# Kernel tuning notes

Hardware: AMD Instinct MI355X
Metric: run time of the kernel (lower is better)

## Reference

```python
import jax, jax.numpy as jnp
import numpy as np

N_NODES = 100000
LATENT_DIM = 8
SAMPLE_SIZE = 8192
N_EDGES = 1000000
EPS = 1e-6


def setup_inputs() -> dict:
    key = jax.random.key(0)
    k1, k2, k3, k4, k5 = jax.random.split(key, 5)
    latent_Z = jax.random.normal(k1, (N_NODES, LATENT_DIM), dtype=jnp.float32)
    alpha = jax.random.normal(k2, (1,), dtype=jnp.float32)
    sample_idx = jax.random.randint(k3, (SAMPLE_SIZE,), 0, N_NODES, dtype=jnp.int64)
    sparse_sample_i = jax.random.randint(k4, (N_EDGES,), 0, N_NODES, dtype=jnp.int64)
    sparse_sample_j = jax.random.randint(k5, (N_EDGES,), 0, N_NODES, dtype=jnp.int64)
    return {"latent_Z": latent_Z, "alpha": alpha, "sample_idx": sample_idx,
            "sparse_sample_i": sparse_sample_i, "sparse_sample_j": sparse_sample_j}


def reference(latent_Z, alpha, sample_idx, sparse_sample_i, sparse_sample_j):
    # --- dense non-edge term over the sampled subgraph ---
    Zs = latent_Z[sample_idx]                              # [S, D]
    diff = Zs[:, None, :] - Zs[None, :, :] + EPS           # [S, S, D]
    dist = jnp.sqrt(jnp.sum(diff * diff, axis=-1))         # [S, S]
    mat = jnp.exp(-dist)                                   # [S, S]
    # original uses exp(ones) vectors in the matmul-with-ones trick -> factor e^2
    ones_exp_sq = jnp.exp(jnp.float32(1.0)) ** 2
    offdiag_sum = jnp.sum(mat) - jnp.sum(jnp.diagonal(mat))
    z_pdist1 = jnp.exp(alpha[0]) * 0.5 * ones_exp_sq * offdiag_sum
    # --- sparse positive-edge term ---
    ed = latent_Z[sparse_sample_i] - latent_Z[sparse_sample_j] + EPS  # [E, D]
    edist = jnp.sqrt(jnp.sum(ed * ed, axis=-1))                        # [E]
    z_pdist2 = jnp.sum(-edist + alpha[0])
    return z_pdist2 - z_pdist1
```

## Files before the change

kernel.cpp:

```cpp
#include <hip/hip_runtime.h>
#include <hip/hip_bf16.h>
#include <math.h>

#define NNODES   100000
#define S        8192
#define D        8
#define EPSF     1e-6f
#define LOG2E    1.442695040888963f
#define EPS_S    (LOG2E * EPSF)
#define NT2      256

#define ZHL_OFF  0
#define U_OFF    262144
#define V_OFF    294912
#define ZB_OFF   327680
#define BK_OFF   1928192

#define NSBLK    256
#define NDBLK    1024
#define NWPP     32
#define CH       6

typedef __attribute__((ext_vector_type(8)))  short short8_t;
typedef __attribute__((ext_vector_type(16))) float f32x16;

__device__ __forceinline__ float block_reduce_f(float v, float* sm) {
    #pragma unroll
    for (int off = 32; off > 0; off >>= 1) v += __shfl_down(v, off, 64);
    int lane = threadIdx.x & 63, wid = threadIdx.x >> 6;
    if (lane == 0) sm[wid] = v;
    __syncthreads();
    float s = 0.f;
    if (threadIdx.x == 0) {
        for (int w = 0; w < 4; ++w) s += sm[w];
    }
    return s;
}

__global__ __launch_bounds__(256) void gather_kernel(const float* __restrict__ Z,
                                                     const int* __restrict__ idx,
                                                     ushort* __restrict__ zhl,
                                                     float* __restrict__ u,
                                                     float* __restrict__ v,
                                                     ushort* __restrict__ zb16,
                                                     char* __restrict__ buckets) {
    int gid = blockIdx.x * 256 + threadIdx.x;

    if (blockIdx.x == 0 && threadIdx.x < 161) {
        *(double*)(buckets + threadIdx.x * 128) = 0.0;
    }

    if (gid < S) {
        int n = idx[gid];
        const float4* zp = (const float4*)(Z + (size_t)n * D);
        float4 a = zp[0], b = zp[1];
        float z[8] = { a.x, a.y, a.z, a.w, b.x, b.y, b.z, b.w };
        float ss = 0.f;
        short8_t h, l;
        #pragma unroll
        for (int k = 0; k < 8; ++k) {
            float zs = LOG2E * z[k];
            ss = fmaf(zs, zs, ss);
            __hip_bfloat16 hb = __float2bfloat16(zs);
            float hf = __bfloat162float(hb);
            __hip_bfloat16 lb = __float2bfloat16(zs - hf);
            h[k] = (short)__builtin_bit_cast(unsigned short, hb);
            l[k] = (short)__builtin_bit_cast(unsigned short, lb);
        }
        *(short8_t*)(zhl + (size_t)gid * 16)     = h;
        *(short8_t*)(zhl + (size_t)gid * 16 + 8) = l;
        u[gid] = ss + 8.f * EPS_S * EPS_S;
        v[gid] = ss;
    }

    if (gid < NNODES) {
        const float4* zp = (const float4*)(Z + (size_t)gid * D);
        float4 a = zp[0], b = zp[1];
        float z[8] = { a.x, a.y, a.z, a.w, b.x, b.y, b.z, b.w };
        short8_t o;
        #pragma unroll
        for (int k = 0; k < 8; ++k) {
            __hip_bfloat16 bb = __float2bfloat16(z[k]);
            o[k] = (short)__builtin_bit_cast(unsigned short, bb);
        }
        *(short8_t*)(zb16 + (size_t)gid * 8) = o;
    }
}

#define UNPACK8(u4, f)                                        \
    f[0] = __uint_as_float(u4.x << 16);                       \
    f[1] = __uint_as_float(u4.x & 0xffff0000u);               \
    f[2] = __uint_as_float(u4.y << 16);                       \
    f[3] = __uint_as_float(u4.y & 0xffff0000u);               \
    f[4] = __uint_as_float(u4.z << 16);                       \
    f[5] = __uint_as_float(u4.z & 0xffff0000u);               \
    f[6] = __uint_as_float(u4.w << 16);                       \
    f[7] = __uint_as_float(u4.w & 0xffff0000u);

__device__ __forceinline__ float edge_dist8(const uint4* __restrict__ zb,
                                            int4 ia0, int4 ia1, int4 ib0, int4 ib1) {
    int aidx[8] = { ia0.x, ia0.y, ia0.z, ia0.w, ia1.x, ia1.y, ia1.z, ia1.w };
    int bidx[8] = { ib0.x, ib0.y, ib0.z, ib0.w, ib1.x, ib1.y, ib1.z, ib1.w };
    uint4 ua[8], ub[8];
    #pragma unroll
    for (int q = 0; q < 8; ++q) { ua[q] = zb[aidx[q]]; ub[q] = zb[bidx[q]]; }
    float acc = 0.f;
    #pragma unroll
    for (int q = 0; q < 8; ++q) {
        float fa[8], fb[8];
        UNPACK8(ua[q], fa);
        UNPACK8(ub[q], fb);
        float s2 = 0.f;
        #pragma unroll
        for (int k = 0; k < 8; ++k) {
            float d = fa[k] - fb[k] + EPSF;
            s2 = fmaf(d, d, s2);
        }
        acc += __builtin_amdgcn_sqrtf(s2);
    }
    return acc;
}

__device__ __forceinline__ void dense_sweep32(const ushort* __restrict__ zhl,
                                              const float* __restrict__ v,
                                              short8_t afrag, const float4* u4,
                                              int ti, int tj0, int cnt, int c31,
                                              float& ax, float& ay, float& az, float& aw) {
    const ushort* bp0 = zhl + (size_t)c31 * 16;
    const float*  vp0 = v + c31;
    for (int t0 = 0; t0 < cnt; t0 += CH) {
        short8_t hh[CH], ll[CH];
        float    vv[CH];
        #pragma unroll
        for (int k = 0; k < CH; ++k) {
            int tk = t0 + k;
            int T  = tj0 + (tk < cnt ? tk : cnt - 1);
            hh[k] = *(const short8_t*)(bp0 + (size_t)T * 512);
            ll[k] = *(const short8_t*)(bp0 + (size_t)T * 512 + 8);
            vv[k] = vp0[T * 32];
        }
        int m = cnt - t0; if (m > CH) m = CH;
        #pragma unroll
        for (int k = 0; k < CH; ++k) {
            if (k < m) {
                float w = (tj0 + t0 + k == ti) ? 1.f : 2.f;
                f32x16 c = { 0.f, 0.f, 0.f, 0.f, 0.f, 0.f, 0.f, 0.f,
                             0.f, 0.f, 0.f, 0.f, 0.f, 0.f, 0.f, 0.f };
                c = __builtin_amdgcn_mfma_f32_32x32x16_bf16(afrag, hh[k], c, 0, 0, 0);
                c = __builtin_amdgcn_mfma_f32_32x32x16_bf16(afrag, ll[k], c, 0, 0, 0);
                #pragma unroll
                for (int q = 0; q < 4; ++q) {
                    float s0 = u4[q].x + vv[k], s1 = u4[q].y + vv[k];
                    float s2 = u4[q].z + vv[k], s3 = u4[q].w + vv[k];
                    float d0 = fmaf(c[4*q+0], -2.f, s0);
                    float d1 = fmaf(c[4*q+1], -2.f, s1);
                    float d2 = fmaf(c[4*q+2], -2.f, s2);
                    float d3 = fmaf(c[4*q+3], -2.f, s3);
                    ax = fmaf(w, __builtin_amdgcn_exp2f(-__builtin_amdgcn_sqrtf(__builtin_fabsf(d0))), ax);
                    ay = fmaf(w, __builtin_amdgcn_exp2f(-__builtin_amdgcn_sqrtf(__builtin_fabsf(d1))), ay);
                    az = fmaf(w, __builtin_amdgcn_exp2f(-__builtin_amdgcn_sqrtf(__builtin_fabsf(d2))), az);
                    aw = fmaf(w, __builtin_amdgcn_exp2f(-__builtin_amdgcn_sqrtf(__builtin_fabsf(d3))), aw);
                }
            }
        }
    }
}

__global__ __launch_bounds__(256) void fused_kernel(
        const ushort* __restrict__ zhl, const float* __restrict__ u,
        const float* __restrict__ v, const ushort* __restrict__ zb16,
        const int* __restrict__ ei, const int* __restrict__ ej, int ne,
        const float* __restrict__ alpha, char* __restrict__ buckets,
        float* __restrict__ out) {
    __shared__ float red[4];
    __shared__ unsigned composeFlag;
    int tid = threadIdx.x, bx = blockIdx.x;
    float s;

    if (bx < NSBLK) {
        const uint4* zb = (const uint4*)zb16;
        const int4* ei4 = (const int4*)ei;
        const int4* ej4 = (const int4*)ej;
        float acc = 0.f;
        int nchunk = ne >> 3;
        int stride = NSBLK * 256;
        int c = bx * 256 + tid;
        if (c < nchunk) {
            int4 ia0 = ei4[2*c], ia1 = ei4[2*c+1];
            int4 ib0 = ej4[2*c], ib1 = ej4[2*c+1];
            while (true) {
                int cn = c + stride;
                bool more = cn < nchunk;
                int4 na0, na1, nb0, nb1;
                if (more) {
                    na0 = ei4[2*cn]; na1 = ei4[2*cn+1];
                    nb0 = ej4[2*cn]; nb1 = ej4[2*cn+1];
                }
                acc += edge_dist8(zb, ia0, ia1, ib0, ib1);
                if (!more) break;
                ia0 = na0; ia1 = na1; ib0 = nb0; ib1 = nb1; c = cn;
            }
        }
        for (int e = (nchunk << 3) + bx * 256 + tid; e < ne; e += stride) {
            uint4 ua = zb[ei[e]];
            uint4 ub = zb[ej[e]];
            float fa[8], fb[8];
            UNPACK8(ua, fa);
            UNPACK8(ub, fb);
            float s2 = 0.f;
            #pragma unroll
            for (int k = 0; k < 8; ++k) {
                float d = fa[k] - fb[k] + EPSF;
                s2 = fmaf(d, d, s2);
            }
            acc += __builtin_amdgcn_sqrtf(s2);
        }
        s = block_reduce_f(acc, red);
    } else {
        int dbx  = bx - NSBLK;
        int wave = tid >> 6, lane = tid & 63;
        int g = lane >> 5, c31 = lane & 31;

        int p  = dbx >> 3;
        int wv = (dbx & 7) * 4 + wave;
        int k0 = (wv * 257) / NWPP;
        int k1 = ((wv + 1) * 257) / NWPP;
        int n1 = NT2 - p;

        float ax = 0.f, ay = 0.f, az = 0.f, aw = 0.f;

        int eA = k1 < n1 ? k1 : n1;
        if (k0 < eA) {
            int ti = p;
            short8_t afrag = *(const short8_t*)(zhl + (size_t)(ti * 32 + c31) * 16 + g * 8);
            float4 u4[4];
            #pragma unroll
            for (int q = 0; q < 4; ++q) u4[q] = *(const float4*)(u + ti * 32 + 8 * q + 4 * g);
            dense_sweep32(zhl, v, afrag, u4, ti, p + k0, eA - k0, c31, ax, ay, az, aw);
        }
        int sB = k0 > n1 ? k0 : n1;
        if (sB < k1) {
            int ti = (NT2 - 1) - p;
            short8_t afrag = *(const short8_t*)(zhl + (size_t)(ti * 32 + c31) * 16 + g * 8);
            float4 u4[4];
            #pragma unroll
            for (int q = 0; q < 4; ++q) u4[q] = *(const float4*)(u + ti * 32 + 8 * q + 4 * g);
            dense_sweep32(zhl, v, afrag, u4, ti, ti + (sB - n1), k1 - sB, c31, ax, ay, az, aw);
        }
        s = block_reduce_f((ax + ay) + (az + aw), red);
    }

    double* dbuck = (double*)(buckets);
    double* sbuck = (double*)(buckets + 64 * 128);
    unsigned* gdone = (unsigned*)(buckets + 160 * 128);

    if (tid == 0) {
        int  sparse = (bx < NSBLK);
        int  sid = sparse ? (bx & 15) : ((bx - NSBLK) & 63);
        int  cid = sparse ? (64 + (bx >> 4)) : ((bx - NSBLK) >> 4);
        double* sumslot = sparse ? (double*)((char*)sbuck + sid * 128)
                                 : (double*)((char*)dbuck + sid * 128);
        (void)atomicAdd(sumslot, (double)s);
        __builtin_amdgcn_s_waitcnt(0);
        unsigned oc = atomicAdd((unsigned*)(buckets + (80 + cid) * 128), 1u);
        unsigned g = 0xFFFFu;
        if (oc == 15u) {
            __builtin_amdgcn_s_waitcnt(0);
            g = atomicAdd(gdone, 1u);
        }
        composeFlag = (g == 79u) ? 1u : 0u;
    }
    __syncthreads();

    if (composeFlag) {
        __shared__ double acc2[2];
        int lane = tid & 63, w = tid >> 6;
        double val = 0.0;
        if (w == 0) val = atomicAdd((double*)((char*)dbuck + lane * 128), 0.0);
        else if (w == 1 && lane < 16) val = atomicAdd((double*)((char*)sbuck + lane * 128), 0.0);
        #pragma unroll
        for (int off = 32; off > 0; off >>= 1) val += __shfl_down(val, off, 64);
        if (w == 0 && lane == 0) acc2[0] = val;
        if (w == 1 && lane == 0) acc2[1] = val;
        __syncthreads();
        if (tid == 0) {
            double Dsum = acc2[0], Ssum = acc2[1];
            double trace = (double)S * exp(-sqrt(8.0) * (double)EPSF);
            double offdiag = Dsum - trace;
            double a = (double)alpha[0];
            double z_pdist2 = (double)ne * a - Ssum;
            double z_pdist1 = exp(a) * 0.5 * 7.3890560989306495 * offdiag;
            out[0] = (float)(z_pdist2 - z_pdist1);
        }
    }
}

extern "C" void kernel_launch(void* const* d_in, const int* in_sizes, int n_in,
                              void* d_out, int out_size, void* d_ws, size_t ws_size,
                              hipStream_t stream) {
    const float* latent_Z = (const float*)d_in[0];
    const float* alpha    = (const float*)d_in[1];
    const int*   sidx     = (const int*)d_in[2];
    const int*   ei       = (const int*)d_in[3];
    const int*   ej       = (const int*)d_in[4];
    int ne = in_sizes[3];
    float* out = (float*)d_out;
    char*  ws  = (char*)d_ws;

    ushort* zhl   = (ushort*)(ws + ZHL_OFF);
    float*  u     = (float*)(ws + U_OFF);
    float*  v     = (float*)(ws + V_OFF);
    ushort* zb16  = (ushort*)(ws + ZB_OFF);
    char*   bk    = ws + BK_OFF;

    gather_kernel<<<(NNODES + 255) / 256, 256, 0, stream>>>(latent_Z, sidx,
                                                            zhl, u, v, zb16, bk);
    fused_kernel<<<NSBLK + NDBLK, 256, 0, stream>>>(zhl, u, v, zb16, ei, ej, ne,
                                                    alpha, bk, out);
}
```

Measured before the change: 31.63 us.

## Split fused sparse/dense kernel into separate launches and simplify dense sweep

The fused kernel that mixed sparse-edge and dense-pair blocks is split into a sparse_kernel with 2048 blocks that writes per-block partials, and a dense_kernel that does the final composition and sums those partials. The dense sweep drops the chunked CH=6 prefetch in favour of a one-ahead software-pipelined loop. The intent is to give the gather-bound sparse term more parallelism, so each thread handles about one chunk, and to shrink the atomic bookkeeping. The cost is an extra kernel launch and serialising the sparse and dense phases, which could no longer overlap.

```diff
diff --git a/kernel.cpp b/kernel.cpp
--- a/kernel.cpp
+++ b/kernel.cpp
@@ -14,12 +14,12 @@
 #define U_OFF    262144
 #define V_OFF    294912
 #define ZB_OFF   327680
-#define BK_OFF   1928192
-
-#define NSBLK    256
+#define SP_OFF   1928192
+#define BK_OFF   1936384
+
+#define NSBLK    2048
 #define NDBLK    1024
 #define NWPP     32
-#define CH       6
 
 typedef __attribute__((ext_vector_type(8)))  short short8_t;
 typedef __attribute__((ext_vector_type(16))) float f32x16;
@@ -46,7 +46,7 @@
                                                      char* __restrict__ buckets) {
     int gid = blockIdx.x * 256 + threadIdx.x;
 
-    if (blockIdx.x == 0 && threadIdx.x < 161) {
+    if (blockIdx.x == 0 && threadIdx.x < 129) {
         *(double*)(buckets + threadIdx.x * 128) = 0.0;
     }
 
@@ -121,163 +121,156 @@
     return acc;
 }
 
+__global__ __launch_bounds__(256) void sparse_kernel(
+        const ushort* __restrict__ zb16, const int* __restrict__ ei,
+        const int* __restrict__ ej, int ne, float* __restrict__ spart) {
+    __shared__ float red[4];
+    int tid = threadIdx.x, bx = blockIdx.x;
+    const uint4* zb = (const uint4*)zb16;
+    const int4* ei4 = (const int4*)ei;
+    const int4* ej4 = (const int4*)ej;
+    float acc = 0.f;
+    int nchunk = ne >> 3;
+    int stride = NSBLK * 256;
+    int c = bx * 256 + tid;
+    if (c < nchunk) {
+        int4 ia0 = ei4[2*c], ia1 = ei4[2*c+1];
+        int4 ib0 = ej4[2*c], ib1 = ej4[2*c+1];
+        while (true) {
+            int cn = c + stride;
+            bool more = cn < nchunk;
+            int4 na0, na1, nb0, nb1;
+            if (more) {
+                na0 = ei4[2*cn]; na1 = ei4[2*cn+1];
+                nb0 = ej4[2*cn]; nb1 = ej4[2*cn+1];
+            }
+            acc += edge_dist8(zb, ia0, ia1, ib0, ib1);
+            if (!more) break;
+            ia0 = na0; ia1 = na1; ib0 = nb0; ib1 = nb1; c = cn;
+        }
+    }
+    for (int e = (nchunk << 3) + bx * 256 + tid; e < ne; e += stride) {
+        uint4 ua = zb[ei[e]];
+        uint4 ub = zb[ej[e]];
+        float fa[8], fb[8];
+        UNPACK8(ua, fa);
+        UNPACK8(ub, fb);
+        float s2 = 0.f;
+        #pragma unroll
+        for (int k = 0; k < 8; ++k) {
+            float d = fa[k] - fb[k] + EPSF;
+            s2 = fmaf(d, d, s2);
+        }
+        acc += __builtin_amdgcn_sqrtf(s2);
+    }
+    float s = block_reduce_f(acc, red);
+    if (tid == 0) spart[bx] = s;
+}
+
 __device__ __forceinline__ void dense_sweep32(const ushort* __restrict__ zhl,
                                               const float* __restrict__ v,
                                               short8_t afrag, const float4* u4,
                                               int ti, int tj0, int cnt, int c31,
                                               float& ax, float& ay, float& az, float& aw) {
-    const ushort* bp0 = zhl + (size_t)c31 * 16;
-    const float*  vp0 = v + c31;
-    for (int t0 = 0; t0 < cnt; t0 += CH) {
-        short8_t hh[CH], ll[CH];
-        float    vv[CH];
-        #pragma unroll
-        for (int k = 0; k < CH; ++k) {
-            int tk = t0 + k;
-            int T  = tj0 + (tk < cnt ? tk : cnt - 1);
-            hh[k] = *(const short8_t*)(bp0 + (size_t)T * 512);
-            ll[k] = *(const short8_t*)(bp0 + (size_t)T * 512 + 8);
-            vv[k] = vp0[T * 32];
-        }
-        int m = cnt - t0; if (m > CH) m = CH;
-        #pragma unroll
-        for (int k = 0; k < CH; ++k) {
-            if (k < m) {
-                float w = (tj0 + t0 + k == ti) ? 1.f : 2.f;
-                f32x16 c = { 0.f, 0.f, 0.f, 0.f, 0.f, 0.f, 0.f, 0.f,
-                             0.f, 0.f, 0.f, 0.f, 0.f, 0.f, 0.f, 0.f };
-                c = __builtin_amdgcn_mfma_f32_32x32x16_bf16(afrag, hh[k], c, 0, 0, 0);
-                c = __builtin_amdgcn_mfma_f32_32x32x16_bf16(afrag, ll[k], c, 0, 0, 0);
-                #pragma unroll
-                for (int q = 0; q < 4; ++q) {
-                    float s0 = u4[q].x + vv[k], s1 = u4[q].y + vv[k];
-                    float s2 = u4[q].z + vv[k], s3 = u4[q].w + vv[k];
-                    float d0 = fmaf(c[4*q+0], -2.f, s0);
-                    float d1 = fmaf(c[4*q+1], -2.f, s1);
-                    float d2 = fmaf(c[4*q+2], -2.f, s2);
-                    float d3 = fmaf(c[4*q+3], -2.f, s3);
-                    ax = fmaf(w, __builtin_amdgcn_exp2f(-__builtin_amdgcn_sqrtf(__builtin_fabsf(d0))), ax);
-                    ay = fmaf(w, __builtin_amdgcn_exp2f(-__builtin_amdgcn_sqrtf(__builtin_fabsf(d1))), ay);
-                    az = fmaf(w, __builtin_amdgcn_exp2f(-__builtin_amdgcn_sqrtf(__builtin_fabsf(d2))), az);
-                    aw = fmaf(w, __builtin_amdgcn_exp2f(-__builtin_amdgcn_sqrtf(__builtin_fabsf(d3))), aw);
-                }
-            }
-        }
-    }
-}
-
-__global__ __launch_bounds__(256) void fused_kernel(
+    const ushort* bp = zhl + (size_t)(tj0 * 32 + c31) * 16;
+    const float*  vp = v + tj0 * 32 + c31;
+    short8_t bh = *(const short8_t*)bp;
+    short8_t bl = *(const short8_t*)(bp + 8);
+    float    vt = vp[0];
+    #pragma unroll 2
+    for (int t = 0; t < cnt; ++t) {
+        short8_t bhc = bh, blc = bl;
+        float    vtc = vt;
+        if (t + 1 < cnt) {
+            bh = *(const short8_t*)(bp + (size_t)(t + 1) * 512);
+            bl = *(const short8_t*)(bp + (size_t)(t + 1) * 512 + 8);
+            vt = vp[(t + 1) * 32];
+        }
+        float w = (tj0 + t == ti) ? 1.f : 2.f;
+        f32x16 c = { 0.f, 0.f, 0.f, 0.f, 0.f, 0.f, 0.f, 0.f,
+                     0.f, 0.f, 0.f, 0.f, 0.f, 0.f, 0.f, 0.f };
+        c = __builtin_amdgcn_mfma_f32_32x32x16_bf16(afrag, bhc, c, 0, 0, 0);
+        c = __builtin_amdgcn_mfma_f32_32x32x16_bf16(afrag, blc, c, 0, 0, 0);
+        #pragma unroll
+        for (int q = 0; q < 4; ++q) {
+            float s0 = u4[q].x + vtc, s1 = u4[q].y + vtc;
+            float s2 = u4[q].z + vtc, s3 = u4[q].w + vtc;
+            float d0 = fmaf(c[4*q+0], -2.f, s0);
+            float d1 = fmaf(c[4*q+1], -2.f, s1);
+            float d2 = fmaf(c[4*q+2], -2.f, s2);
+            float d3 = fmaf(c[4*q+3], -2.f, s3);
+            ax = fmaf(w, __builtin_amdgcn_exp2f(-__builtin_amdgcn_sqrtf(__builtin_fabsf(d0))), ax);
+            ay = fmaf(w, __builtin_amdgcn_exp2f(-__builtin_amdgcn_sqrtf(__builtin_fabsf(d1))), ay);
+            az = fmaf(w, __builtin_amdgcn_exp2f(-__builtin_amdgcn_sqrtf(__builtin_fabsf(d2))), az);
+            aw = fmaf(w, __builtin_amdgcn_exp2f(-__builtin_amdgcn_sqrtf(__builtin_fabsf(d3))), aw);
+        }
+    }
+}
+
+__global__ __launch_bounds__(256) void dense_kernel(
         const ushort* __restrict__ zhl, const float* __restrict__ u,
-        const float* __restrict__ v, const ushort* __restrict__ zb16,
-        const int* __restrict__ ei, const int* __restrict__ ej, int ne,
-        const float* __restrict__ alpha, char* __restrict__ buckets,
-        float* __restrict__ out) {
+        const float* __restrict__ v, const float* __restrict__ alpha,
+        const float* __restrict__ spart, char* __restrict__ buckets,
+        float* __restrict__ out, int ne) {
     __shared__ float red[4];
     __shared__ unsigned composeFlag;
     int tid = threadIdx.x, bx = blockIdx.x;
-    float s;
-
-    if (bx < NSBLK) {
-        const uint4* zb = (const uint4*)zb16;
-        const int4* ei4 = (const int4*)ei;
-        const int4* ej4 = (const int4*)ej;
-        float acc = 0.f;
-        int nchunk = ne >> 3;
-        int stride = NSBLK * 256;
-        int c = bx * 256 + tid;
-        if (c < nchunk) {
-            int4 ia0 = ei4[2*c], ia1 = ei4[2*c+1];
-            int4 ib0 = ej4[2*c], ib1 = ej4[2*c+1];
-            while (true) {
-                int cn = c + stride;
-                bool more = cn < nchunk;
-                int4 na0, na1, nb0, nb1;
-                if (more) {
-                    na0 = ei4[2*cn]; na1 = ei4[2*cn+1];
-                    nb0 = ej4[2*cn]; nb1 = ej4[2*cn+1];
-                }
-                acc += edge_dist8(zb, ia0, ia1, ib0, ib1);
-                if (!more) break;
-                ia0 = na0; ia1 = na1; ib0 = nb0; ib1 = nb1; c = cn;
-            }
-        }
-        for (int e = (nchunk << 3) + bx * 256 + tid; e < ne; e += stride) {
-            uint4 ua = zb[ei[e]];
-            uint4 ub = zb[ej[e]];
-            float fa[8], fb[8];
-            UNPACK8(ua, fa);
-            UNPACK8(ub, fb);
-            float s2 = 0.f;
-            #pragma unroll
-            for (int k = 0; k < 8; ++k) {
-                float d = fa[k] - fb[k] + EPSF;
-                s2 = fmaf(d, d, s2);
-            }
-            acc += __builtin_amdgcn_sqrtf(s2);
-        }
-        s = block_reduce_f(acc, red);
-    } else {
-        int dbx  = bx - NSBLK;
-        int wave = tid >> 6, lane = tid & 63;
-        int g = lane >> 5, c31 = lane & 31;
-
-        int p  = dbx >> 3;
-        int wv = (dbx & 7) * 4 + wave;
-        int k0 = (wv * 257) / NWPP;
-        int k1 = ((wv + 1) * 257) / NWPP;
-        int n1 = NT2 - p;
-
-        float ax = 0.f, ay = 0.f, az = 0.f, aw = 0.f;
-
-        int eA = k1 < n1 ? k1 : n1;
-        if (k0 < eA) {
-            int ti = p;
-            short8_t afrag = *(const short8_t*)(zhl + (size_t)(ti * 32 + c31) * 16 + g * 8);
-            float4 u4[4];
-            #pragma unroll
-            for (int q = 0; q < 4; ++q) u4[q] = *(const float4*)(u + ti * 32 + 8 * q + 4 * g);
-            dense_sweep32(zhl, v, afrag, u4, ti, p + k0, eA - k0, c31, ax, ay, az, aw);
-        }
-        int sB = k0 > n1 ? k0 : n1;
-        if (sB < k1) {
-            int ti = (NT2 - 1) - p;
-            short8_t afrag = *(const short8_t*)(zhl + (size_t)(ti * 32 + c31) * 16 + g * 8);
-            float4 u4[4];
-            #pragma unroll
-            for (int q = 0; q < 4; ++q) u4[q] = *(const float4*)(u + ti * 32 + 8 * q + 4 * g);
-            dense_sweep32(zhl, v, afrag, u4, ti, ti + (sB - n1), k1 - sB, c31, ax, ay, az, aw);
-        }
-        s = block_reduce_f((ax + ay) + (az + aw), red);
-    }
+    int wave = tid >> 6, lane = tid & 63;
+    int g = lane >> 5, c31 = lane & 31;
+
+    int p  = bx >> 3;
+    int wv = (bx & 7) * 4 + wave;
+    int k0 = (wv * 257) / NWPP;
+    int k1 = ((wv + 1) * 257) / NWPP;
+    int n1 = NT2 - p;
+
+    float ax = 0.f, ay = 0.f, az = 0.f, aw = 0.f;
+
+    int eA = k1 < n1 ? k1 : n1;
+    if (k0 < eA) {
+        int ti = p;
+        short8_t afrag = *(const short8_t*)(zhl + (size_t)(ti * 32 + c31) * 16 + g * 8);
+        float4 u4[4];
+        #pragma unroll
+        for (int q = 0; q < 4; ++q) u4[q] = *(const float4*)(u + ti * 32 + 8 * q + 4 * g);
+        dense_sweep32(zhl, v, afrag, u4, ti, p + k0, eA - k0, c31, ax, ay, az, aw);
+    }
+    int sB = k0 > n1 ? k0 : n1;
+    if (sB < k1) {
+        int ti = (NT2 - 1) - p;
+        short8_t afrag = *(const short8_t*)(zhl + (size_t)(ti * 32 + c31) * 16 + g * 8);
+        float4 u4[4];
+        #pragma unroll
+        for (int q = 0; q < 4; ++q) u4[q] = *(const float4*)(u + ti * 32 + 8 * q + 4 * g);
+        dense_sweep32(zhl, v, afrag, u4, ti, ti + (sB - n1), k1 - sB, c31, ax, ay, az, aw);
+    }
+    float s = block_reduce_f((ax + ay) + (az + aw), red);
 
     double* dbuck = (double*)(buckets);
-    double* sbuck = (double*)(buckets + 64 * 128);
-    unsigned* gdone = (unsigned*)(buckets + 160 * 128);
+    unsigned* gdone = (unsigned*)(buckets + 128 * 128);
 
     if (tid == 0) {
-        int  sparse = (bx < NSBLK);
-        int  sid = sparse ? (bx & 15) : ((bx - NSBLK) & 63);
-        int  cid = sparse ? (64 + (bx >> 4)) : ((bx - NSBLK) >> 4);
-        double* sumslot = sparse ? (double*)((char*)sbuck + sid * 128)
-                                 : (double*)((char*)dbuck + sid * 128);
-        (void)atomicAdd(sumslot, (double)s);
+        int b = bx & 63;
+        (void)atomicAdd((double*)((char*)dbuck + b * 128), (double)s);
         __builtin_amdgcn_s_waitcnt(0);
-        unsigned oc = atomicAdd((unsigned*)(buckets + (80 + cid) * 128), 1u);
-        unsigned g = 0xFFFFu;
+        unsigned oc = atomicAdd((unsigned*)(buckets + (64 + b) * 128), 1u);
+        unsigned gg = 0xFFFFu;
         if (oc == 15u) {
             __builtin_amdgcn_s_waitcnt(0);
-            g = atomicAdd(gdone, 1u);
-        }
-        composeFlag = (g == 79u) ? 1u : 0u;
+            gg = atomicAdd(gdone, 1u);
+        }
+        composeFlag = (gg == 63u) ? 1u : 0u;
     }
     __syncthreads();
 
     if (composeFlag) {
         __shared__ double acc2[2];
-        int lane = tid & 63, w = tid >> 6;
+        int w = tid >> 6;
         double val = 0.0;
         if (w == 0) val = atomicAdd((double*)((char*)dbuck + lane * 128), 0.0);
-        else if (w == 1 && lane < 16) val = atomicAdd((double*)((char*)sbuck + lane * 128), 0.0);
+        else if (w == 1) {
+            for (int k = lane; k < NSBLK; k += 64) val += (double)spart[k];
+        }
         #pragma unroll
         for (int off = 32; off > 0; off >>= 1) val += __shfl_down(val, off, 64);
         if (w == 0 && lane == 0) acc2[0] = val;
@@ -311,10 +304,11 @@
     float*  u     = (float*)(ws + U_OFF);
     float*  v     = (float*)(ws + V_OFF);
     ushort* zb16  = (ushort*)(ws + ZB_OFF);
+    float*  spart = (float*)(ws + SP_OFF);
     char*   bk    = ws + BK_OFF;
 
     gather_kernel<<<(NNODES + 255) / 256, 256, 0, stream>>>(latent_Z, sidx,
                                                             zhl, u, v, zb16, bk);
-    fused_kernel<<<NSBLK + NDBLK, 256, 0, stream>>>(zhl, u, v, zb16, ei, ej, ne,
-                                                    alpha, bk, out);
-}
+    sparse_kernel<<<NSBLK, 256, 0, stream>>>(zb16, ei, ej, ne, spart);
+    dense_kernel<<<NDBLK, 256, 0, stream>>>(zhl, u, v, alpha, spart, bk, out, ne);
+}
```

New measurement: 40.90 us. 1.29x slower.

## Drop bf16 hi/lo split for dense Gram term; single MFMA with zero-padded K

Applied to the files above, without the earlier changes.

Replaces the two-MFMA hi+lo bf16 split of the scaled latent vectors with a single bf16 representation. The squared norms are now computed from the rounded values, so the distance identity stays consistent with the rounded dot products. The upper half of K for the B operand points at a zero row instead of the lo part. The sweep loop becomes a one-step software-prefetched loop instead of batched CH=6 loads. This halves MFMA work and B-operand traffic, at the cost of bf16 rounding error in the distances.

```diff
diff --git a/kernel.cpp b/kernel.cpp
--- a/kernel.cpp
+++ b/kernel.cpp
@@ -10,16 +10,16 @@
 #define EPS_S    (LOG2E * EPSF)
 #define NT2      256
 
-#define ZHL_OFF  0
-#define U_OFF    262144
-#define V_OFF    294912
-#define ZB_OFF   327680
-#define BK_OFF   1928192
+#define ZBS_OFF  0
+#define U_OFF    131104
+#define V_OFF    163872
+#define ZB_OFF   196640
+#define BK_OFF   1796736
 
 #define NSBLK    256
 #define NDBLK    1024
 #define NWPP     32
-#define CH       6
+#define ZROW     8192
 
 typedef __attribute__((ext_vector_type(8)))  short short8_t;
 typedef __attribute__((ext_vector_type(16))) float f32x16;
@@ -39,7 +39,7 @@
 
 __global__ __launch_bounds__(256) void gather_kernel(const float* __restrict__ Z,
                                                      const int* __restrict__ idx,
-                                                     ushort* __restrict__ zhl,
+                                                     ushort* __restrict__ zbs,
                                                      float* __restrict__ u,
                                                      float* __restrict__ v,
                                                      ushort* __restrict__ zb16,
@@ -48,6 +48,10 @@
 
     if (blockIdx.x == 0 && threadIdx.x < 161) {
         *(double*)(buckets + threadIdx.x * 128) = 0.0;
+    }
+    if (blockIdx.x == 0 && threadIdx.x == 200) {
+        short8_t zz = { 0,0,0,0,0,0,0,0 };
+        *(short8_t*)(zbs + (size_t)ZROW * 8) = zz;
     }
 
     if (gid < S) {
@@ -56,19 +60,16 @@
         float4 a = zp[0], b = zp[1];
         float z[8] = { a.x, a.y, a.z, a.w, b.x, b.y, b.z, b.w };
         float ss = 0.f;
-        short8_t h, l;
+        short8_t h;
         #pragma unroll
         for (int k = 0; k < 8; ++k) {
             float zs = LOG2E * z[k];
-            ss = fmaf(zs, zs, ss);
             __hip_bfloat16 hb = __float2bfloat16(zs);
             float hf = __bfloat162float(hb);
-            __hip_bfloat16 lb = __float2bfloat16(zs - hf);
+            ss = fmaf(hf, hf, ss);
             h[k] = (short)__builtin_bit_cast(unsigned short, hb);
-            l[k] = (short)__builtin_bit_cast(unsigned short, lb);
-        }
-        *(short8_t*)(zhl + (size_t)gid * 16)     = h;
-        *(short8_t*)(zhl + (size_t)gid * 16 + 8) = l;
+        }
+        *(short8_t*)(zbs + (size_t)gid * 8) = h;
         u[gid] = ss + 8.f * EPS_S * EPS_S;
         v[gid] = ss;
     }
@@ -121,53 +122,46 @@
     return acc;
 }
 
-__device__ __forceinline__ void dense_sweep32(const ushort* __restrict__ zhl,
+__device__ __forceinline__ void dense_sweep32(const ushort* __restrict__ zbs,
                                               const float* __restrict__ v,
                                               short8_t afrag, const float4* u4,
-                                              int ti, int tj0, int cnt, int c31,
+                                              int ti, int tj0, int cnt, int c31, int g,
                                               float& ax, float& ay, float& az, float& aw) {
-    const ushort* bp0 = zhl + (size_t)c31 * 16;
-    const float*  vp0 = v + c31;
-    for (int t0 = 0; t0 < cnt; t0 += CH) {
-        short8_t hh[CH], ll[CH];
-        float    vv[CH];
-        #pragma unroll
-        for (int k = 0; k < CH; ++k) {
-            int tk = t0 + k;
-            int T  = tj0 + (tk < cnt ? tk : cnt - 1);
-            hh[k] = *(const short8_t*)(bp0 + (size_t)T * 512);
-            ll[k] = *(const short8_t*)(bp0 + (size_t)T * 512 + 8);
-            vv[k] = vp0[T * 32];
-        }
-        int m = cnt - t0; if (m > CH) m = CH;
-        #pragma unroll
-        for (int k = 0; k < CH; ++k) {
-            if (k < m) {
-                float w = (tj0 + t0 + k == ti) ? 1.f : 2.f;
-                f32x16 c = { 0.f, 0.f, 0.f, 0.f, 0.f, 0.f, 0.f, 0.f,
-                             0.f, 0.f, 0.f, 0.f, 0.f, 0.f, 0.f, 0.f };
-                c = __builtin_amdgcn_mfma_f32_32x32x16_bf16(afrag, hh[k], c, 0, 0, 0);
-                c = __builtin_amdgcn_mfma_f32_32x32x16_bf16(afrag, ll[k], c, 0, 0, 0);
-                #pragma unroll
-                for (int q = 0; q < 4; ++q) {
-                    float s0 = u4[q].x + vv[k], s1 = u4[q].y + vv[k];
-                    float s2 = u4[q].z + vv[k], s3 = u4[q].w + vv[k];
-                    float d0 = fmaf(c[4*q+0], -2.f, s0);
-                    float d1 = fmaf(c[4*q+1], -2.f, s1);
-                    float d2 = fmaf(c[4*q+2], -2.f, s2);
-                    float d3 = fmaf(c[4*q+3], -2.f, s3);
-                    ax = fmaf(w, __builtin_amdgcn_exp2f(-__builtin_amdgcn_sqrtf(__builtin_fabsf(d0))), ax);
-                    ay = fmaf(w, __builtin_amdgcn_exp2f(-__builtin_amdgcn_sqrtf(__builtin_fabsf(d1))), ay);
-                    az = fmaf(w, __builtin_amdgcn_exp2f(-__builtin_amdgcn_sqrtf(__builtin_fabsf(d2))), az);
-                    aw = fmaf(w, __builtin_amdgcn_exp2f(-__builtin_amdgcn_sqrtf(__builtin_fabsf(d3))), aw);
-                }
-            }
+    const ushort* bp = zbs + (size_t)(g ? ZROW : (tj0 * 32 + c31)) * 8;
+    size_t step = g ? 0 : 256;
+    const float* vp = v + tj0 * 32 + c31;
+    short8_t bnext = *(const short8_t*)bp;
+    float    vnext = vp[0];
+    #pragma unroll 4
+    for (int t = 0; t < cnt; ++t) {
+        short8_t bc = bnext;
+        float    vtc = vnext;
+        if (t + 1 < cnt) {
+            bnext = *(const short8_t*)(bp + (size_t)(t + 1) * step);
+            vnext = vp[(t + 1) * 32];
+        }
+        float w = (tj0 + t == ti) ? 1.f : 2.f;
+        f32x16 c = { 0.f, 0.f, 0.f, 0.f, 0.f, 0.f, 0.f, 0.f,
+                     0.f, 0.f, 0.f, 0.f, 0.f, 0.f, 0.f, 0.f };
+        c = __builtin_amdgcn_mfma_f32_32x32x16_bf16(afrag, bc, c, 0, 0, 0);
+        #pragma unroll
+        for (int q = 0; q < 4; ++q) {
+            float s0 = u4[q].x + vtc, s1 = u4[q].y + vtc;
+            float s2 = u4[q].z + vtc, s3 = u4[q].w + vtc;
+            float d0 = fmaf(c[4*q+0], -2.f, s0);
+            float d1 = fmaf(c[4*q+1], -2.f, s1);
+            float d2 = fmaf(c[4*q+2], -2.f, s2);
+            float d3 = fmaf(c[4*q+3], -2.f, s3);
+            ax = fmaf(w, __builtin_amdgcn_exp2f(-__builtin_amdgcn_sqrtf(__builtin_fabsf(d0))), ax);
+            ay = fmaf(w, __builtin_amdgcn_exp2f(-__builtin_amdgcn_sqrtf(__builtin_fabsf(d1))), ay);
+            az = fmaf(w, __builtin_amdgcn_exp2f(-__builtin_amdgcn_sqrtf(__builtin_fabsf(d2))), az);
+            aw = fmaf(w, __builtin_amdgcn_exp2f(-__builtin_amdgcn_sqrtf(__builtin_fabsf(d3))), aw);
         }
     }
 }
 
 __global__ __launch_bounds__(256) void fused_kernel(
-        const ushort* __restrict__ zhl, const float* __restrict__ u,
+        const ushort* __restrict__ zbs, const float* __restrict__ u,
         const float* __restrict__ v, const ushort* __restrict__ zb16,
         const int* __restrict__ ei, const int* __restrict__ ej, int ne,
         const float* __restrict__ alpha, char* __restrict__ buckets,
@@ -232,20 +226,20 @@
         int eA = k1 < n1 ? k1 : n1;
         if (k0 < eA) {
             int ti = p;
-            short8_t afrag = *(const short8_t*)(zhl + (size_t)(ti * 32 + c31) * 16 + g * 8);
+            short8_t afrag = *(const short8_t*)(zbs + (size_t)(ti * 32 + c31) * 8);
             float4 u4[4];
             #pragma unroll
             for (int q = 0; q < 4; ++q) u4[q] = *(const float4*)(u + ti * 32 + 8 * q + 4 * g);
-            dense_sweep32(zhl, v, afrag, u4, ti, p + k0, eA - k0, c31, ax, ay, az, aw);
+            dense_sweep32(zbs, v, afrag, u4, ti, p + k0, eA - k0, c31, g, ax, ay, az, aw);
         }
         int sB = k0 > n1 ? k0 : n1;
         if (sB < k1) {
             int ti = (NT2 - 1) - p;
-            short8_t afrag = *(const short8_t*)(zhl + (size_t)(ti * 32 + c31) * 16 + g * 8);
+            short8_t afrag = *(const short8_t*)(zbs + (size_t)(ti * 32 + c31) * 8);
             float4 u4[4];
             #pragma unroll
             for (int q = 0; q < 4; ++q) u4[q] = *(const float4*)(u + ti * 32 + 8 * q + 4 * g);
-            dense_sweep32(zhl, v, afrag, u4, ti, ti + (sB - n1), k1 - sB, c31, ax, ay, az, aw);
+            dense_sweep32(zbs, v, afrag, u4, ti, ti + (sB - n1), k1 - sB, c31, g, ax, ay, az, aw);
         }
         s = block_reduce_f((ax + ay) + (az + aw), red);
     }
@@ -307,14 +301,14 @@
     float* out = (float*)d_out;
     char*  ws  = (char*)d_ws;
 
-    ushort* zhl   = (ushort*)(ws + ZHL_OFF);
+    ushort* zbs   = (ushort*)(ws + ZBS_OFF);
     float*  u     = (float*)(ws + U_OFF);
     float*  v     = (float*)(ws + V_OFF);
     ushort* zb16  = (ushort*)(ws + ZB_OFF);
     char*   bk    = ws + BK_OFF;
 
     gather_kernel<<<(NNODES + 255) / 256, 256, 0, stream>>>(latent_Z, sidx,
-                                                            zhl, u, v, zb16, bk);
-    fused_kernel<<<NSBLK + NDBLK, 256, 0, stream>>>(zhl, u, v, zb16, ei, ej, ne,
+                                                            zbs, u, v, zb16, bk);
+    fused_kernel<<<NSBLK + NDBLK, 256, 0, stream>>>(zbs, u, v, zb16, ei, ej, ne,
                                                     alpha, bk, out);
 }
```

New measurement: 30.84 us. 1.03x faster.
